# Optimization experiments

Measured on AMD Instinct MI355X. Metric: run time of the kernel, lower is better.

## Reference

```python
import jax, jax.numpy as jnp
import numpy as np

D = 64          # embedding_dim
B = 1024        # batch (queries)
R = 128         # num_relations
N = 100000      # num_nodes
E = 6400000     # num_edges


def setup_inputs() -> dict:
    key = jax.random.key(0)
    ks = jax.random.split(key, 16)
    inp = {
        "relation_embeddings": jax.random.normal(ks[0], (B, R, D), dtype=jnp.float32),
        "query_rels": jax.random.randint(ks[1], (B,), 0, R),
        "query_entities": jax.random.randint(ks[2], (B,), 0, N),
        "edge_index": jax.random.randint(ks[3], (2, E), 0, N),
        "edge_type": jax.random.randint(ks[4], (E,), 0, R),
        "num_nodes": N,
        # feature_extractor: Linear(2D+4 -> D), ReLU, Linear(D -> D//2), ReLU
        "W1": jax.random.normal(ks[5], (2 * D + 4, D), dtype=jnp.float32) * 0.05,
        "b1": jnp.zeros((D,), dtype=jnp.float32),
        "W2": jax.random.normal(ks[6], (D, D // 2), dtype=jnp.float32) * 0.05,
        "b2": jnp.zeros((D // 2,), dtype=jnp.float32),
        # gate_network: Linear(D//2 -> D//4), ReLU, Linear(D//4 -> 1), Sigmoid
        "Wg1": jax.random.normal(ks[7], (D // 2, D // 4), dtype=jnp.float32) * 0.05,
        "bg1": jnp.zeros((D // 4,), dtype=jnp.float32),
        "Wg2": jax.random.normal(ks[8], (D // 4, 1), dtype=jnp.float32) * 0.05,
        "bg2": jnp.full((1,), 0.85, dtype=jnp.float32),
    }
    return inp


def reference(relation_embeddings, query_rels, query_entities, edge_index,
              edge_type, num_nodes, W1, b1, W2, b2, Wg1, bg1, Wg2, bg2):
    b, r, d = relation_embeddings.shape
    e = edge_type.shape[0]
    e_f = jnp.float32(e)
    src, dst = edge_index[0], edge_index[1]
    # count self-loop edges once (matches boolean OR mask in torch code)
    not_loop = (src != dst).astype(jnp.float32)

    # --- graph statistics (vectorized replacement of per-query masks) ---
    rel_counts = jnp.zeros((r,), jnp.float32).at[edge_type].add(1.0)          # [R]
    rel_freq_norm = jnp.minimum(rel_counts[query_rels] / e_f, 1.0)            # [B]

    deg = (jnp.zeros((num_nodes,), jnp.float32)
           .at[src].add(1.0).at[dst].add(not_loop))                           # [N]
    deg_q = deg[query_entities]                                               # [B]
    entity_degree_norm = jnp.minimum(deg_q / e_f, 1.0)

    density = jnp.minimum(e_f / jnp.float32(num_nodes * num_nodes), 1.0)
    stats = jnp.stack([rel_freq_norm, entity_degree_norm, rel_freq_norm,
                       jnp.full_like(rel_freq_norm, density)], axis=-1)       # [B,4]

    # --- query relation embedding ---
    rel_emb = relation_embeddings[jnp.arange(b), query_rels]                  # [B,D]

    # --- entity embedding = mean of relation embeddings over incident edges ---
    # per-node histogram of incident edge types (self loops counted once)
    hist = (jnp.zeros((num_nodes, r), jnp.float32)
            .at[src, edge_type].add(1.0)
            .at[dst, edge_type].add(not_loop))                                # [N,R]
    Mq = hist[query_entities]                                                 # [B,R]
    ent_sum = jnp.einsum('br,brd->bd', Mq, relation_embeddings)               # [B,D]
    entity_emb = ent_sum / jnp.maximum(deg_q, 1.0)[:, None]                   # zeros if deg==0

    # --- gated MLP ---
    feat = jnp.concatenate([rel_emb, entity_emb, stats], axis=-1)             # [B,2D+4]
    h = jax.nn.relu(feat @ W1 + b1)
    h = jax.nn.relu(h @ W2 + b2)
    g = jax.nn.relu(h @ Wg1 + bg1)
    gate = jax.nn.sigmoid(g @ Wg2 + bg2)[:, 0]                                # [B]
    return gate
```

## Files before the change

kernel.cpp:

```cpp
#include <hip/hip_runtime.h>
#include <math.h>


#define NNODES 100000
#define NWORDS ((NNODES + 31) / 32)
#define NWP    (((NWORDS + 3) / 4) * 4)
#define RR     128
#define DD     64
#define FF     (2 * DD + 4)
#define E4C    1600000
#define EDGE_BLOCKS 512
#define NTC    (EDGE_BLOCKS * 1024)
#define HITCAP 2048

__global__ void __launch_bounds__(1024)
setup_kernel(const int* __restrict__ qents, int B,
             unsigned* __restrict__ gmask, int* __restrict__ gbase,
             int4* __restrict__ zp, int n4)
{
    int t = threadIdx.x;
    if (blockIdx.x != 0) {
        int i = (blockIdx.x - 1) * 1024 + t;
        int stride = (gridDim.x - 1) * 1024;
        int4 z = make_int4(0, 0, 0, 0);
        for (int k = i; k < n4; k += stride) zp[k] = z;
        return;
    }
    __shared__ unsigned s_mask[NWP];
    __shared__ int s_wsum[16], s_wbase[16];
    for (int k = t; k < NWP; k += 1024) s_mask[k] = 0u;
    __syncthreads();
    for (int b = t; b < B; b += 1024) {
        int e = qents[b];
        atomicOr(&s_mask[e >> 5], 1u << (e & 31));
    }
    __syncthreads();
    int w0 = t * 4;
    int pc[4]; int sum = 0;
#pragma unroll
    for (int k = 0; k < 4; ++k) {
        int w = w0 + k;
        unsigned mm = (w < NWP) ? s_mask[w] : 0u;
        pc[k] = __popc(mm);
        sum += pc[k];
    }
    int lane = t & 63, wid = t >> 6;
    int incl = sum;
#pragma unroll
    for (int off = 1; off < 64; off <<= 1) {
        int v = __shfl_up(incl, off);
        if (lane >= off) incl += v;
    }
    if (lane == 63) s_wsum[wid] = incl;
    __syncthreads();
    if (t == 0) {
        int run = 0;
#pragma unroll
        for (int k = 0; k < 16; ++k) { s_wbase[k] = run; run += s_wsum[k]; }
    }
    __syncthreads();
    int base = s_wbase[wid] + incl - sum;
#pragma unroll
    for (int k = 0; k < 4; ++k) {
        int w = w0 + k;
        if (w < NWP) gbase[w] = base;
        base += pc[k];
    }
    for (int k = t; k < NWP; k += 1024) gmask[k] = s_mask[k];
}

static __device__ __forceinline__ void edge1(
    int s, int d, int ty, int* s_cnt,
    const unsigned* s_mask, const int* s_base,
    unsigned* s_hit, int* s_hn, int* __restrict__ Mslot)
{
    atomicAdd(&s_cnt[ty], 1);
    unsigned ws = s_mask[s >> 5];
    if ((ws >> (s & 31)) & 1u) {
        int slot = s_base[s >> 5] + __popc(ws & ((1u << (s & 31)) - 1u));
        int idx = atomicAdd(s_hn, 1);
        if (idx < HITCAP) s_hit[idx] = (unsigned)(slot * RR + ty);
        else atomicAdd(&Mslot[slot * RR + ty], 1);
    }
    if (s != d) {
        unsigned wd = s_mask[d >> 5];
        if ((wd >> (d & 31)) & 1u) {
            int slot = s_base[d >> 5] + __popc(wd & ((1u << (d & 31)) - 1u));
            int idx = atomicAdd(s_hn, 1);
            if (idx < HITCAP) s_hit[idx] = (unsigned)(slot * RR + ty);
            else atomicAdd(&Mslot[slot * RR + ty], 1);
        }
    }
}

static __device__ __forceinline__ void edge4(
    int4 s, int4 d, int4 ty, int* s_cnt,
    const unsigned* s_mask, const int* s_base,
    unsigned* s_hit, int* s_hn, int* __restrict__ Mslot)
{
    edge1(s.x, d.x, ty.x, s_cnt, s_mask, s_base, s_hit, s_hn, Mslot);
    edge1(s.y, d.y, ty.y, s_cnt, s_mask, s_base, s_hit, s_hn, Mslot);
    edge1(s.z, d.z, ty.z, s_cnt, s_mask, s_base, s_hit, s_hn, Mslot);
    edge1(s.w, d.w, ty.w, s_cnt, s_mask, s_base, s_hit, s_hn, Mslot);
}

__global__ void __launch_bounds__(1024, 8)
edge_kernel(const int* __restrict__ ei, const int* __restrict__ etype,
            int E, int E4,
            const unsigned* __restrict__ gmask, const int* __restrict__ gbase,
            int* __restrict__ Mslot, int* __restrict__ relcnt)
{
    __shared__ int s_cnt[RR];
    __shared__ __align__(16) unsigned s_mask[NWP];
    __shared__ __align__(16) int s_base[NWP];
    __shared__ unsigned s_hit[HITCAP];
    __shared__ int s_hn;
    int t = threadIdx.x;
    if (t < RR) s_cnt[t] = 0;
    if (t == 0) s_hn = 0;
    const uint4* gm4 = (const uint4*)gmask;
    const int4*  gb4 = (const int4*)gbase;
    for (int i = t; i < NWP / 4; i += 1024) {
        ((uint4*)s_mask)[i] = gm4[i];
        ((int4*)s_base)[i]  = gb4[i];
    }
    __syncthreads();

    int tid  = blockIdx.x * 1024 + t;
    int nthr = gridDim.x * 1024;

    const int4* src4 = (const int4*)ei;
    const int4* dst4 = (const int4*)(ei + E);
    const int4* et4  = (const int4*)etype;

    if (E4 == E4C && nthr == NTC) {
        int i0 = tid, i1 = tid + NTC, i2 = tid + 2 * NTC;
        int4 sa = src4[i0], da = dst4[i0], ta = et4[i0];
        int4 sb = src4[i1], db = dst4[i1], tb = et4[i1];
        int4 sc = src4[i2], dc = dst4[i2], tc = et4[i2];
        edge4(sa, da, ta, s_cnt, s_mask, s_base, s_hit, &s_hn, Mslot);
        edge4(sb, db, tb, s_cnt, s_mask, s_base, s_hit, &s_hn, Mslot);
        edge4(sc, dc, tc, s_cnt, s_mask, s_base, s_hit, &s_hn, Mslot);
        int i3 = tid + 3 * NTC;
        if (i3 < E4C) {
            int4 sd = src4[i3], dd = dst4[i3], td = et4[i3];
            edge4(sd, dd, td, s_cnt, s_mask, s_base, s_hit, &s_hn, Mslot);
        }
    } else {
        for (int i = tid; i < E4; i += nthr) {
            int4 s = src4[i], d = dst4[i], ty = et4[i];
            edge4(s, d, ty, s_cnt, s_mask, s_base, s_hit, &s_hn, Mslot);
        }
        for (int e = (E4 << 2) + tid; e < E; e += nthr)
            edge1(ei[e], ei[E + e], etype[e], s_cnt, s_mask, s_base,
                  s_hit, &s_hn, Mslot);
    }

    __syncthreads();
    int hn = s_hn; if (hn > HITCAP) hn = HITCAP;
    for (int i = t; i < hn; i += 1024)
        atomicAdd(&Mslot[s_hit[i]], 1);
    if (t < RR) {
        int c = s_cnt[t];
        if (c) atomicAdd(&relcnt[t], c);
    }
}

__global__ void query_kernel(
    const float* __restrict__ RE,
    const int* __restrict__ qrels, const int* __restrict__ qents,
    const int* __restrict__ relcnt, const int* __restrict__ Mslot,
    const unsigned* __restrict__ gmask, const int* __restrict__ gbase,
    const float* __restrict__ W1, const float* __restrict__ b1,
    const float* __restrict__ W2, const float* __restrict__ b2,
    const float* __restrict__ Wg1, const float* __restrict__ bg1,
    const float* __restrict__ Wg2, const float* __restrict__ bg2,
    float* __restrict__ out, float e_f, float density)
{
    __shared__ float s_m[RR];
    __shared__ float s_part[256];
    __shared__ float s_feat[FF];
    __shared__ float s_h1[DD];
    __shared__ float s_h2[DD / 2];
    __shared__ float s_g[DD / 4];
    __shared__ int s_slot;

    int b = blockIdx.x;
    int t = threadIdx.x;
    int d = t & (DD - 1);
    int w = t >> 6;

    if (t == 0) {
        int e = qents[b];
        unsigned mm = gmask[e >> 5];
        s_slot = gbase[e >> 5] + __popc(mm & ((1u << (e & 31)) - 1u));
    }
    __syncthreads();
    int slot = s_slot;

    if (t < RR) s_m[t] = (float)Mslot[slot * RR + t];
    __syncthreads();

    const float* REb = RE + (size_t)b * RR * DD;
    float acc = 0.f;
#pragma unroll 4
    for (int r = w; r < RR; r += 4) {
        float m = s_m[r];
        if (m != 0.f) acc = fmaf(m, REb[r * DD + d], acc);
    }
    s_part[w * DD + d] = acc;
    __syncthreads();

    if (t < DD) {
        float ds = s_m[t] + s_m[t + DD];
#pragma unroll
        for (int off = 32; off > 0; off >>= 1) ds += __shfl_xor(ds, off);

        float ent = s_part[t] + s_part[DD + t] + s_part[2 * DD + t] + s_part[3 * DD + t];

        int qr = qrels[b];
        s_feat[t]      = REb[qr * DD + t];
        s_feat[DD + t] = ent / fmaxf(ds, 1.f);
        if (t == 0) {
            float rf = fminf((float)relcnt[qr] / e_f, 1.f);
            s_feat[2 * DD + 0] = rf;
            s_feat[2 * DD + 1] = fminf(ds / e_f, 1.f);
            s_feat[2 * DD + 2] = rf;
            s_feat[2 * DD + 3] = density;
        }
    }
    __syncthreads();

    {
        int c = t >> 6, n = t & 63;
        int i0 = c * 33;
        float a = 0.f;
#pragma unroll
        for (int k = 0; k < 33; ++k) {
            int i = i0 + k;
            a = fmaf(s_feat[i], W1[i * DD + n], a);
        }
        s_part[t] = a;
    }
    __syncthreads();
    if (t < DD) {
        float a = b1[t] + s_part[t] + s_part[64 + t] + s_part[128 + t] + s_part[192 + t];
        s_h1[t] = fmaxf(a, 0.f);
    }
    __syncthreads();

    {
        int c = t >> 5, n = t & 31;
        float a = 0.f;
#pragma unroll
        for (int k = 0; k < 8; ++k) {
            int i = c * 8 + k;
            a = fmaf(s_h1[i], W2[i * 32 + n], a);
        }
        s_part[t] = a;
    }
    __syncthreads();
    if (t < 32) {
        float a = b2[t];
#pragma unroll
        for (int c = 0; c < 8; ++c) a += s_part[c * 32 + t];
        s_h2[t] = fmaxf(a, 0.f);
    }
    __syncthreads();

    if (t < 16) {
        float a = bg1[t];
#pragma unroll
        for (int i = 0; i < 32; ++i) a = fmaf(s_h2[i], Wg1[i * 16 + t], a);
        s_g[t] = fmaxf(a, 0.f);
    }
    __syncthreads();

    if (t == 0) {
        float a = bg2[0];
#pragma unroll
        for (int i = 0; i < 16; ++i) a = fmaf(s_g[i], Wg2[i], a);
        out[b] = 1.f / (1.f + expf(-a));
    }
}

extern "C" void kernel_launch(void* const* d_in, const int* in_sizes, int n_in,
                              void* d_out, int out_size, void* d_ws, size_t ws_size,
                              hipStream_t stream)
{
    const float* RE    = (const float*)d_in[0];
    const int*   qrels = (const int*)d_in[1];
    const int*   qents = (const int*)d_in[2];
    const int*   ei    = (const int*)d_in[3];
    const int*   etype = (const int*)d_in[4];
    const float* W1  = (const float*)d_in[6];
    const float* b1  = (const float*)d_in[7];
    const float* W2  = (const float*)d_in[8];
    const float* b2  = (const float*)d_in[9];
    const float* Wg1 = (const float*)d_in[10];
    const float* bg1 = (const float*)d_in[11];
    const float* Wg2 = (const float*)d_in[12];
    const float* bg2 = (const float*)d_in[13];
    float* out = (float*)d_out;

    int B = in_sizes[1];
    int E = in_sizes[4];

    int* ws_i   = (int*)d_ws;
    int* Mslot  = ws_i;
    int* relcnt = Mslot + (size_t)B * RR;
    unsigned* mask = (unsigned*)(relcnt + RR);
    int* word_base = (int*)(mask + NWP);

    float e_f = (float)E;
    float density = fminf((float)E / ((float)NNODES * (float)NNODES), 1.f);

    int n4 = (B * RR + RR) / 4;

    setup_kernel<<<64, 1024, 0, stream>>>(qents, B, mask, word_base,
                                          (int4*)d_ws, n4);

    int E4 = ((E & 3) == 0) ? (E >> 2) : 0;
    edge_kernel<<<EDGE_BLOCKS, 1024, 0, stream>>>(ei, etype, E, E4,
                                                  mask, word_base,
                                                  Mslot, relcnt);

    query_kernel<<<B, 256, 0, stream>>>(RE, qrels, qents, relcnt, Mslot,
                                        mask, word_base,
                                        W1, b1, W2, b2, Wg1, bg1, Wg2, bg2,
                                        out, e_f, density);
}
```

Measured before the change: 48.03 us.

## Move relation counting into setup kernel and defer edge-type loads to hits

```diff
diff --git a/kernel.cpp b/kernel.cpp
--- a/kernel.cpp
+++ b/kernel.cpp
@@ -12,18 +12,39 @@
 #define EDGE_BLOCKS 512
 #define NTC    (EDGE_BLOCKS * 1024)
 #define HITCAP 2048
+#define SETUP_BLOCKS 256
 
 __global__ void __launch_bounds__(1024)
 setup_kernel(const int* __restrict__ qents, int B,
              unsigned* __restrict__ gmask, int* __restrict__ gbase,
-             int4* __restrict__ zp, int n4)
+             const int* __restrict__ etype, int E,
+             int* __restrict__ relcnt)
 {
     int t = threadIdx.x;
     if (blockIdx.x != 0) {
+        __shared__ int s_cnt[RR];
+        if (t < RR) s_cnt[t] = 0;
+        __syncthreads();
+        int ne4 = E >> 2;
+        const int4* et4 = (const int4*)etype;
         int i = (blockIdx.x - 1) * 1024 + t;
-        int stride = (gridDim.x - 1) * 1024;
-        int4 z = make_int4(0, 0, 0, 0);
-        for (int k = i; k < n4; k += stride) zp[k] = z;
+        int stride = (SETUP_BLOCKS - 1) * 1024;
+        for (int k = i; k < ne4; k += stride) {
+            int4 ty = et4[k];
+            atomicAdd(&s_cnt[ty.x], 1);
+            atomicAdd(&s_cnt[ty.y], 1);
+            atomicAdd(&s_cnt[ty.z], 1);
+            atomicAdd(&s_cnt[ty.w], 1);
+        }
+        if (blockIdx.x == 1) {
+            for (int e = (ne4 << 2) + t; e < E; e += 1024)
+                atomicAdd(&s_cnt[etype[e]], 1);
+        }
+        __syncthreads();
+        if (t < RR) {
+            int c = s_cnt[t];
+            if (c) atomicAdd(&relcnt[t], c);
+        }
         return;
     }
     __shared__ unsigned s_mask[NWP];
@@ -69,54 +90,72 @@
     for (int k = t; k < NWP; k += 1024) gmask[k] = s_mask[k];
 }
 
-static __device__ __forceinline__ void edge1(
-    int s, int d, int ty, int* s_cnt,
+static __device__ __forceinline__ void hitrec(
+    int node, int e,
     const unsigned* s_mask, const int* s_base,
-    unsigned* s_hit, int* s_hn, int* __restrict__ Mslot)
-{
-    atomicAdd(&s_cnt[ty], 1);
+    unsigned short* s_hslot, unsigned* s_hedge, int* s_hn,
+    int* __restrict__ Mslot, const int* __restrict__ etype)
+{
+    unsigned w = s_mask[node >> 5];
+    if ((w >> (node & 31)) & 1u) {
+        int slot = s_base[node >> 5] + __popc(w & ((1u << (node & 31)) - 1u));
+        int idx = atomicAdd(s_hn, 1);
+        if (idx < HITCAP) {
+            s_hslot[idx] = (unsigned short)slot;
+            s_hedge[idx] = (unsigned)e;
+        } else {
+            atomicAdd(&Mslot[slot * RR + etype[e]], 1);
+        }
+    }
+}
+
+static __device__ __forceinline__ void edge4s(
+    int4 s, int4 d, int i,
+    const unsigned* s_mask, const int* s_base,
+    unsigned short* s_hslot, unsigned* s_hedge, int* s_hn,
+    int* __restrict__ Mslot, const int* __restrict__ etype)
+{
+    int e = i * 4;
+    hitrec(s.x, e + 0, s_mask, s_base, s_hslot, s_hedge, s_hn, Mslot, etype);
+    if (s.x != d.x) hitrec(d.x, e + 0, s_mask, s_base, s_hslot, s_hedge, s_hn, Mslot, etype);
+    hitrec(s.y, e + 1, s_mask, s_base, s_hslot, s_hedge, s_hn, Mslot, etype);
+    if (s.y != d.y) hitrec(d.y, e + 1, s_mask, s_base, s_hslot, s_hedge, s_hn, Mslot, etype);
+    hitrec(s.z, e + 2, s_mask, s_base, s_hslot, s_hedge, s_hn, Mslot, etype);
+    if (s.z != d.z) hitrec(d.z, e + 2, s_mask, s_base, s_hslot, s_hedge, s_hn, Mslot, etype);
+    hitrec(s.w, e + 3, s_mask, s_base, s_hslot, s_hedge, s_hn, Mslot, etype);
+    if (s.w != d.w) hitrec(d.w, e + 3, s_mask, s_base, s_hslot, s_hedge, s_hn, Mslot, etype);
+}
+
+static __device__ __forceinline__ void edge1g(
+    int s, int d, int ty,
+    const unsigned* s_mask, const int* s_base, int* __restrict__ Mslot)
+{
     unsigned ws = s_mask[s >> 5];
     if ((ws >> (s & 31)) & 1u) {
         int slot = s_base[s >> 5] + __popc(ws & ((1u << (s & 31)) - 1u));
-        int idx = atomicAdd(s_hn, 1);
-        if (idx < HITCAP) s_hit[idx] = (unsigned)(slot * RR + ty);
-        else atomicAdd(&Mslot[slot * RR + ty], 1);
+        atomicAdd(&Mslot[slot * RR + ty], 1);
     }
     if (s != d) {
         unsigned wd = s_mask[d >> 5];
         if ((wd >> (d & 31)) & 1u) {
             int slot = s_base[d >> 5] + __popc(wd & ((1u << (d & 31)) - 1u));
-            int idx = atomicAdd(s_hn, 1);
-            if (idx < HITCAP) s_hit[idx] = (unsigned)(slot * RR + ty);
-            else atomicAdd(&Mslot[slot * RR + ty], 1);
-        }
-    }
-}
-
-static __device__ __forceinline__ void edge4(
-    int4 s, int4 d, int4 ty, int* s_cnt,
-    const unsigned* s_mask, const int* s_base,
-    unsigned* s_hit, int* s_hn, int* __restrict__ Mslot)
-{
-    edge1(s.x, d.x, ty.x, s_cnt, s_mask, s_base, s_hit, s_hn, Mslot);
-    edge1(s.y, d.y, ty.y, s_cnt, s_mask, s_base, s_hit, s_hn, Mslot);
-    edge1(s.z, d.z, ty.z, s_cnt, s_mask, s_base, s_hit, s_hn, Mslot);
-    edge1(s.w, d.w, ty.w, s_cnt, s_mask, s_base, s_hit, s_hn, Mslot);
+            atomicAdd(&Mslot[slot * RR + ty], 1);
+        }
+    }
 }
 
 __global__ void __launch_bounds__(1024, 8)
 edge_kernel(const int* __restrict__ ei, const int* __restrict__ etype,
             int E, int E4,
             const unsigned* __restrict__ gmask, const int* __restrict__ gbase,
-            int* __restrict__ Mslot, int* __restrict__ relcnt)
-{
-    __shared__ int s_cnt[RR];
+            int* __restrict__ Mslot)
+{
     __shared__ __align__(16) unsigned s_mask[NWP];
     __shared__ __align__(16) int s_base[NWP];
-    __shared__ unsigned s_hit[HITCAP];
+    __shared__ unsigned s_hedge[HITCAP];
+    __shared__ unsigned short s_hslot[HITCAP];
     __shared__ int s_hn;
     int t = threadIdx.x;
-    if (t < RR) s_cnt[t] = 0;
     if (t == 0) s_hn = 0;
     const uint4* gm4 = (const uint4*)gmask;
     const int4*  gb4 = (const int4*)gbase;
@@ -131,38 +170,39 @@
 
     const int4* src4 = (const int4*)ei;
     const int4* dst4 = (const int4*)(ei + E);
-    const int4* et4  = (const int4*)etype;
 
     if (E4 == E4C && nthr == NTC) {
         int i0 = tid, i1 = tid + NTC, i2 = tid + 2 * NTC;
-        int4 sa = src4[i0], da = dst4[i0], ta = et4[i0];
-        int4 sb = src4[i1], db = dst4[i1], tb = et4[i1];
-        int4 sc = src4[i2], dc = dst4[i2], tc = et4[i2];
-        edge4(sa, da, ta, s_cnt, s_mask, s_base, s_hit, &s_hn, Mslot);
-        edge4(sb, db, tb, s_cnt, s_mask, s_base, s_hit, &s_hn, Mslot);
-        edge4(sc, dc, tc, s_cnt, s_mask, s_base, s_hit, &s_hn, Mslot);
+        int4 sa = src4[i0], da = dst4[i0];
+        int4 sb = src4[i1], db = dst4[i1];
+        int4 sc = src4[i2], dc = dst4[i2];
+        edge4s(sa, da, i0, s_mask, s_base, s_hslot, s_hedge, &s_hn, Mslot, etype);
+        edge4s(sb, db, i1, s_mask, s_base, s_hslot, s_hedge, &s_hn, Mslot, etype);
+        edge4s(sc, dc, i2, s_mask, s_base, s_hslot, s_hedge, &s_hn, Mslot, etype);
         int i3 = tid + 3 * NTC;
         if (i3 < E4C) {
-            int4 sd = src4[i3], dd = dst4[i3], td = et4[i3];
-            edge4(sd, dd, td, s_cnt, s_mask, s_base, s_hit, &s_hn, Mslot);
+            int4 sd = src4[i3], dd = dst4[i3];
+            edge4s(sd, dd, i3, s_mask, s_base, s_hslot, s_hedge, &s_hn, Mslot, etype);
         }
     } else {
+        const int4* et4 = (const int4*)etype;
         for (int i = tid; i < E4; i += nthr) {
             int4 s = src4[i], d = dst4[i], ty = et4[i];
-            edge4(s, d, ty, s_cnt, s_mask, s_base, s_hit, &s_hn, Mslot);
+            edge1g(s.x, d.x, ty.x, s_mask, s_base, Mslot);
+            edge1g(s.y, d.y, ty.y, s_mask, s_base, Mslot);
+            edge1g(s.z, d.z, ty.z, s_mask, s_base, Mslot);
+            edge1g(s.w, d.w, ty.w, s_mask, s_base, Mslot);
         }
         for (int e = (E4 << 2) + tid; e < E; e += nthr)
-            edge1(ei[e], ei[E + e], etype[e], s_cnt, s_mask, s_base,
-                  s_hit, &s_hn, Mslot);
+            edge1g(ei[e], ei[E + e], etype[e], s_mask, s_base, Mslot);
     }
 
     __syncthreads();
     int hn = s_hn; if (hn > HITCAP) hn = HITCAP;
-    for (int i = t; i < hn; i += 1024)
-        atomicAdd(&Mslot[s_hit[i]], 1);
-    if (t < RR) {
-        int c = s_cnt[t];
-        if (c) atomicAdd(&relcnt[t], c);
+    for (int i = t; i < hn; i += 1024) {
+        int e  = (int)s_hedge[i];
+        int ty = etype[e];
+        atomicAdd(&Mslot[(int)s_hslot[i] * RR + ty], 1);
     }
 }
 
@@ -315,15 +355,14 @@
     float e_f = (float)E;
     float density = fminf((float)E / ((float)NNODES * (float)NNODES), 1.f);
 
-    int n4 = (B * RR + RR) / 4;
-
-    setup_kernel<<<64, 1024, 0, stream>>>(qents, B, mask, word_base,
-                                          (int4*)d_ws, n4);
+    hipMemsetAsync(d_ws, 0, ((size_t)B * RR + RR) * sizeof(int), stream);
+
+    setup_kernel<<<SETUP_BLOCKS, 1024, 0, stream>>>(qents, B, mask, word_base,
+                                                    etype, E, relcnt);
 
     int E4 = ((E & 3) == 0) ? (E >> 2) : 0;
     edge_kernel<<<EDGE_BLOCKS, 1024, 0, stream>>>(ei, etype, E, E4,
-                                                  mask, word_base,
-                                                  Mslot, relcnt);
+                                                  mask, word_base, Mslot);
 
     query_kernel<<<B, 256, 0, stream>>>(RE, qrels, qents, relcnt, Mslot,
                                         mask, word_base,
```

After: 46.03 us. -4.2%, faster.
